# Kernel tuning notes

Hardware: AMD Instinct MI355X
Metric: run time of the kernel (lower is better)

Reference implementation:

```python
import jax, jax.numpy as jnp
import numpy as np

H = 16      # query heads
KV = 8      # kv heads
D = 128     # head_dim
HID = 2048  # hidden_size
T = 2048    # tokens
EPS = 1e-6
THETA = 1000000.0


def setup_inputs() -> dict:
    key = jax.random.key(0)
    ks = jax.random.split(key, 4)
    return {
        "hidden_states": jax.random.normal(ks[0], (T, HID), jnp.float32),
        "positions": jnp.arange(T, dtype=jnp.int32),
        "qkv_w": jax.random.normal(ks[1], (H * D + 2 * KV * D, HID), jnp.float32) * 0.02,
        "o_w": jax.random.normal(ks[2], (HID, H * D), jnp.float32) * 0.02,
        "q_norm_w": jnp.ones((D,), jnp.float32),
        "k_norm_w": jnp.ones((D,), jnp.float32),
    }


def _rmsnorm(x, w):
    # x: [T, heads, D]; normalize over last dim
    var = jnp.mean(x * x, axis=-1, keepdims=True)
    return x * jax.lax.rsqrt(var + EPS) * w


def _rope(x, positions):
    # neox-style rotate-half; x: [T, heads, D]
    half = D // 2
    inv_freq = 1.0 / (THETA ** (jnp.arange(0, half, dtype=jnp.float32) / half * 1.0))
    inv_freq = 1.0 / (THETA ** (jnp.arange(0, D, 2, dtype=jnp.float32) / D))
    ang = positions.astype(jnp.float32)[:, None] * inv_freq  # [T, D/2]
    cos = jnp.cos(ang)[:, None, :]
    sin = jnp.sin(ang)[:, None, :]
    x1, x2 = x[..., :half], x[..., half:]
    return jnp.concatenate([x1 * cos - x2 * sin, x2 * cos + x1 * sin], axis=-1)


def reference(hidden_states, positions, qkv_w, o_w, q_norm_w, k_norm_w):
    scale = D ** -0.5
    qkv = hidden_states @ qkv_w.T  # [T, H*D + 2*KV*D]
    q = qkv[:, : H * D].reshape(T, H, D)
    k = qkv[:, H * D : H * D + KV * D].reshape(T, KV, D)
    v = qkv[:, H * D + KV * D :].reshape(T, KV, D)

    q = _rope(_rmsnorm(q, q_norm_w), positions)
    k = _rope(_rmsnorm(k, k_norm_w), positions)

    # GQA: repeat kv heads to match query heads
    rep = H // KV
    k = jnp.repeat(k, rep, axis=1)  # [T, H, D]
    v = jnp.repeat(v, rep, axis=1)

    scores = jnp.einsum("thd,shd->hts", q, k) * scale  # [H, T, T]
    causal = positions[:, None] >= positions[None, :]  # [T, T]
    scores = jnp.where(causal[None, :, :], scores, jnp.float32(-1e30))
    p = jax.nn.softmax(scores, axis=-1)
    o = jnp.einsum("hts,shd->thd", p, v).reshape(T, H * D)
    return o @ o_w.T  # [T, HID]
```

## Files before the change

kernel.cpp:

```cpp
#include <hip/hip_runtime.h>
#include <math.h>

#define T_TOK 2048
#define HID 2048
#define NH 16
#define NKV 8
#define HD 128
#define QKV_N 4096
#define EPS 1e-6f

typedef unsigned short u16;
typedef unsigned int   u32;
typedef __attribute__((ext_vector_type(8))) u16   u16x8;
typedef __attribute__((ext_vector_type(8))) short short8;
typedef __attribute__((ext_vector_type(4))) float floatx4;
typedef __attribute__((ext_vector_type(16))) float f32x16;
typedef __attribute__((ext_vector_type(4))) u32   u32x4;

__device__ __forceinline__ u16 f2bf(float x) {
    u32 u = __float_as_uint(x);
    u = (u + 0x7fffu + ((u >> 16) & 1u)) >> 16;
    return (u16)u;
}
__device__ __forceinline__ float bf2f(u16 h) {
    return __uint_as_float(((u32)h) << 16);
}
__device__ __forceinline__ u32 cvtpk_bf16(float lo, float hi) {
    u32 r;
    asm("v_cvt_pk_bf16_f32 %0, %1, %2" : "=v"(r) : "v"(lo), "v"(hi));
    return r;
}

__device__ __forceinline__ void cvt8(const float* __restrict__ in,
                                     u16* __restrict__ out, size_t i)
{
    float4 a = *(const float4*)(in + i);
    float4 b = *(const float4*)(in + i + 4);
    u16x8 o;
    o[0] = f2bf(a.x); o[1] = f2bf(a.y); o[2] = f2bf(a.z); o[3] = f2bf(a.w);
    o[4] = f2bf(b.x); o[5] = f2bf(b.y); o[6] = f2bf(b.z); o[7] = f2bf(b.w);
    *(u16x8*)(out + i) = o;
}

__global__ __launch_bounds__(256) void cvt_pair(
    const float* __restrict__ ina, u16* __restrict__ outa,
    const float* __restrict__ inb, u16* __restrict__ outb)
{
    const int bid = blockIdx.x;
    if (bid < 2048) cvt8(ina, outa, ((size_t)bid * 256 + threadIdx.x) * 8);
    else            cvt8(inb, outb, ((size_t)(bid - 2048) * 256 + threadIdx.x) * 8);
}

#define GBM 256
#define GBN 128
#define GBK 64
#define BUFSH 24576

#define WAITV6 asm volatile("s_waitcnt vmcnt(6)" ::: "memory")
#define WAITV0 asm volatile("s_waitcnt vmcnt(0)" ::: "memory")
#define LGKM0  asm volatile("s_waitcnt lgkmcnt(0)" ::: "memory")
#define BARR   asm volatile("s_barrier" ::: "memory")
#define SB     __builtin_amdgcn_sched_barrier(0)

#define STAGEU(i, tt, dstb) \
    __builtin_amdgcn_global_load_lds( \
        (const __attribute__((address_space(1))) u32*)(gsrc[i] + (size_t)(tt)*GBK), \
        (__attribute__((address_space(3))) u32*)((dstb) + loff[i]), 16, 0, 0)

#define RD_A(dst, srcb, f) do { \
    dst[0] = *(const short8*)((srcb) + arow + (f)*1024 + achunk0); \
    dst[1] = *(const short8*)((srcb) + arow + (f)*1024 + achunk1); } while (0)

#define RD_B(dst, srcb) do { \
    _Pragma("unroll") \
    for (int j_ = 0; j_ < 4; ++j_) { \
        dst[j_][0] = *(const short8*)((srcb) + 16384 + brow + j_*1024 + achunk0); \
        dst[j_][1] = *(const short8*)((srcb) + 16384 + brow + j_*1024 + achunk1); } } while (0)

#define MM(f, aa, bb) do { \
    __builtin_amdgcn_s_setprio(1); \
    _Pragma("unroll") \
    for (int j_ = 0; j_ < 4; ++j_) { \
        acc[f][j_] = __builtin_amdgcn_mfma_f32_16x16x32_bf16(aa[0], bb[j_][0], acc[f][j_], 0, 0, 0); \
        acc[f][j_] = __builtin_amdgcn_mfma_f32_16x16x32_bf16(aa[1], bb[j_][1], acc[f][j_], 0, 0, 0); } \
    __builtin_amdgcn_s_setprio(0); } while (0)

#define TILE(t, CURB, NXTB, THDB, BBC, BBN) do { \
    const bool st_ = (t) + 2 < nt; \
    if (st_) { STAGEU(0, (t)+2, THDB); STAGEU(1, (t)+2, THDB); } \
    RD_A(aP1, CURB, 1); SB; \
    MM(0, aP0, BBC); SB; \
    if (st_) { STAGEU(2, (t)+2, THDB); STAGEU(3, (t)+2, THDB); } \
    RD_A(aP0, CURB, 2); SB; \
    MM(1, aP1, BBC); SB; \
    if (st_) { STAGEU(4, (t)+2, THDB); STAGEU(5, (t)+2, THDB); } \
    RD_A(aP1, CURB, 3); SB; \
    MM(2, aP0, BBC); \
    if ((t) + 1 < nt) { \
        if (st_) { WAITV6; } else { WAITV0; } \
        LGKM0; BARR; SB; \
        RD_B(BBN, NXTB); RD_A(aP0, NXTB, 0); \
    } \
    SB; \
    MM(3, aP1, BBC); SB; \
} while (0)

template<bool OUT_BF16>
__global__ __launch_bounds__(512, 2) void gemm_bt_8p(
    const u16* __restrict__ A, const u16* __restrict__ B,
    void* __restrict__ Cv, int K, int lda, int ldb, int ldc)
{
    extern __shared__ short lds[];
    const int tid = threadIdx.x;
    const int w  = tid >> 6;
    const int l  = tid & 63;
    const int m0 = blockIdx.y * GBM;
    const int n0 = blockIdx.x * GBN;
    const int mr = (w >> 1) * 64;
    const int nc = (w & 1) * 64;
    const int cc = l & 15;
    const int q4 = l >> 4;

    const int lr = l >> 3;
    const int gchunk = ((l & 7) ^ (lr & 7)) * 8;
    const u16* gsrc[6]; int loff[6];
    #pragma unroll
    for (int i = 0; i < 6; ++i) {
        const int u = w * 6 + i;
        if (u < 32) {
            gsrc[i] = A + (size_t)(m0 + u*8 + lr) * lda + gchunk;
            loff[i] = u * 512;
        } else {
            const int v = u - 32;
            gsrc[i] = B + (size_t)(n0 + v*8 + lr) * ldb + gchunk;
            loff[i] = 16384 + v * 512;
        }
    }

    const int achunk0 = ((q4)     ^ (cc & 7)) * 8;
    const int achunk1 = ((4 + q4) ^ (cc & 7)) * 8;
    const int arow = (mr + cc) * 64;
    const int brow = (nc + cc) * 64;

    floatx4 acc[4][4];
    #pragma unroll
    for (int f = 0; f < 4; ++f)
        #pragma unroll
        for (int j = 0; j < 4; ++j) acc[f][j] = (floatx4){0.f, 0.f, 0.f, 0.f};

    short8 aP0[2], aP1[2], bbE[4][2], bbO[4][2];
    short* b0 = lds;
    short* b1 = lds + BUFSH;
    short* b2 = lds + 2 * BUFSH;
    const int nt = K >> 6;

    #pragma unroll
    for (int i = 0; i < 6; ++i) STAGEU(i, 0, b0);
    #pragma unroll
    for (int i = 0; i < 6; ++i) STAGEU(i, 1, b1);
    WAITV6; BARR; SB;
    RD_B(bbE, b0); RD_A(aP0, b0, 0);

    short *CURB = b0, *NXTB = b1, *THDB = b2;
    for (int t = 0; t < nt; t += 2) {
        TILE(t, CURB, NXTB, THDB, bbE, bbO);
        { short* tmp = CURB; CURB = NXTB; NXTB = THDB; THDB = tmp; }
        TILE(t + 1, CURB, NXTB, THDB, bbO, bbE);
        { short* tmp = CURB; CURB = NXTB; NXTB = THDB; THDB = tmp; }
    }

    const int r0 = q4 * 4;
    #pragma unroll
    for (int f = 0; f < 4; ++f)
        #pragma unroll
        for (int j = 0; j < 4; ++j)
            #pragma unroll
            for (int r = 0; r < 4; ++r) {
                const int row = m0 + mr + f*16 + r0 + r;
                const int col = n0 + nc + j*16 + cc;
                if (OUT_BF16)
                    ((u16*)Cv)[(size_t)row * ldc + col] = f2bf(acc[f][j][r]);
                else
                    ((float*)Cv)[(size_t)row * ldc + col] = acc[f][j][r];
            }
}

__global__ __launch_bounds__(256) void prep_cvt(
    u16* __restrict__ qkv, const int* __restrict__ positions,
    const float* __restrict__ qw, const float* __restrict__ kw,
    u16* __restrict__ Kp, u16* __restrict__ Vtp,
    const float* __restrict__ ow, u16* __restrict__ owbf)
{
    const int bid = blockIdx.x;
    if (bid >= 256) {
        cvt8(ow, owbf, ((size_t)(bid - 256) * 256 + threadIdx.x) * 8);
        return;
    }
    const int tile = bid & 31, kvh = bid >> 5;
    const int tid = threadIdx.x;
    const int w = tid >> 6, l = tid & 63;
    const int t0 = tile * 64;

    const float qw0 = qw[2*l], qw1 = qw[2*l+1];
    const float kw0 = kw[2*l], kw1 = kw[2*l+1];
    const int   i0  = (2*l) & 63;
    const float if0 = exp2f(-(float)i0     * 0.311430758895690f);
    const float if1 = exp2f(-(float)(i0+1) * 0.311430758895690f);

    for (int rr = w; rr < 64; rr += 4) {
        const int t = t0 + rr;
        const int pos = positions[t];
        const float a0 = (float)pos * if0;
        const float a1 = (float)pos * if1;
        const float s0 = sinf(a0), c0 = cosf(a0);
        const float s1 = sinf(a1), c1 = cosf(a1);

        #pragma unroll
        for (int pass = 0; pass < 3; ++pass) {
            const int off = (pass < 2) ? (2*kvh + pass)*HD : NH*HD + kvh*HD;
            const float w0 = (pass < 2) ? qw0 : kw0;
            const float w1 = (pass < 2) ? qw1 : kw1;
            u16* p = qkv + (size_t)t*QKV_N + off;

            const u32 pk = *(const u32*)(p + 2*l);
            const float x0 = bf2f((u16)pk), x1 = bf2f((u16)(pk >> 16));
            float ss = x0*x0 + x1*x1;
            #pragma unroll
            for (int x = 1; x < 64; x <<= 1) ss += __shfl_xor(ss, x);
            const float rs = rsqrtf(ss * (1.0f/128.0f) + EPS);
            const float xn0 = x0 * rs * w0, xn1 = x1 * rs * w1;
            const float px0 = __shfl_xor(xn0, 32);
            const float px1 = __shfl_xor(xn1, 32);

            float o0, o1;
            if (l < 32) { o0 = xn0*c0 - px0*s0; o1 = xn1*c1 - px1*s1; }
            else        { o0 = xn0*c0 + px0*s0; o1 = xn1*c1 + px1*s1; }
            const u32 outpk = (u32)f2bf(o0) | ((u32)f2bf(o1) << 16);

            if (pass < 2) {
                *(u32*)(p + 2*l) = outpk;
            } else {
                const int ch = l >> 2;
                u16* dst = Kp + ((size_t)(kvh*32 + tile)*64 + rr)*128
                              + (ch ^ (rr & 15))*8 + (l & 3)*2;
                *(u32*)dst = outpk;
            }
        }
    }

    __shared__ u16 tl[64][136];
    {
        const int t  = tid >> 2;
        const int c0 = (tid & 3) * 32;
        const u16* src = qkv + (size_t)(t0 + t)*QKV_N + NH*HD + NKV*HD + kvh*HD + c0;
        #pragma unroll
        for (int p2 = 0; p2 < 4; ++p2)
            *(u16x8*)(&tl[t][c0 + p2*8]) = *(const u16x8*)(src + p2*8);
    }
    __syncthreads();
    {
        u16* dstb = Vtp + (size_t)(kvh*32 + tile) * 128 * 64;
        #pragma unroll
        for (int i = 0; i < 4; ++i) {
            const int id = tid*4 + i;
            const int d = id >> 3;
            const int o = id & 7;
            const int sb = (o ^ (d & 7)) * 8;
            u16x8 v;
            #pragma unroll
            for (int j = 0; j < 8; ++j) v[j] = tl[sb + j][d];
            *(u16x8*)(dstb + d*64 + o*8) = v;
        }
    }
}

__global__ __launch_bounds__(256, 2) void attn_mfma32(
    const u16* __restrict__ qkv, const u16* __restrict__ Kp,
    const u16* __restrict__ Vtp,
    u16* __restrict__ Opart, float2* __restrict__ ml)
{
    const int id   = blockIdx.x;
    const int kvh  = id & 7;
    const int u    = id >> 3;
    const int half = u >> 5;
    const int v    = u & 31;
    const int hp   = v & 1;
    const int bq   = v >> 1;
    const int qt   = half ? bq : 15 - bq;
    const int h    = kvh*2 + hp;
    const int t0q  = qt * 128;

    const int tid = threadIdx.x;
    const int w   = tid >> 6;
    const int l   = tid & 63;
    const int q31 = l & 31;
    const int hi  = l >> 5;

    __shared__ short Ks[2][8192];
    __shared__ short Vts[2][8192];

    short8 qf[8];
    {
        const u16* qrow = qkv + (size_t)(t0q + w*32 + q31) * QKV_N + h*HD;
        #pragma unroll
        for (int ks = 0; ks < 8; ++ks)
            qf[ks] = *(const short8*)(qrow + ks*16 + hi*8);
    }

    float m_run = -3.0e38f, l_run = 0.f;
    f32x16 accO[4];
    #pragma unroll
    for (int nd = 0; nd < 4; ++nd)
        #pragma unroll
        for (int r = 0; r < 16; ++r) accO[nd][r] = 0.f;

    const float Cs = 0.12751744f;

    const int nt  = 2*qt + 2;
    const int nh0 = qt + 1;
    const int tlo = half ? nh0 : 0;
    const int thi = half ? nt  : nh0;

    auto issue = [&](int tile, int buf) {
        const size_t tb = (size_t)(kvh*32 + tile) * 8192;
        const u16* g = ((w < 2) ? Kp : Vtp) + tb + (w & 1)*4096 + l*8;
        short* p = ((w < 2) ? Ks[buf] : Vts[buf]) + (w & 1)*4096 + l*8;
        #pragma unroll
        for (int i = 0; i < 8; ++i)
            __builtin_amdgcn_global_load_lds(
                (const __attribute__((address_space(1))) u32*)(g + i*512),
                (__attribute__((address_space(3))) u32*)(p + i*512), 16, 0, 0);
    };

    issue(tlo, 0);
    int cur = 0;

    for (int tile = tlo; tile < thi; ++tile) {
        __syncthreads();
        if (tile + 1 < thi) issue(tile + 1, cur ^ 1);

        const short* Kc = Ks[cur];
        const short* Vc = Vts[cur];

        f32x16 accS0, accS1;
        #pragma unroll
        for (int r = 0; r < 16; ++r) { accS0[r] = 0.f; accS1[r] = 0.f; }

        __builtin_amdgcn_s_setprio(1);
        #pragma unroll
        for (int ks = 0; ks < 8; ++ks) {
            const int pc = ((2*ks + hi) ^ (q31 & 15)) * 8;
            short8 a0 = *(const short8*)(Kc + q31*128 + pc);
            short8 a1 = *(const short8*)(Kc + (32 + q31)*128 + pc);
            accS0 = __builtin_amdgcn_mfma_f32_32x32x16_bf16(a0, qf[ks], accS0, 0, 0, 0);
            accS1 = __builtin_amdgcn_mfma_f32_32x32x16_bf16(a1, qf[ks], accS1, 0, 0, 0);
        }
        __builtin_amdgcn_s_setprio(0);

        if (tile >= 2*qt) {
            const int qg = w*32 + q31 + t0q - tile*64;
            #pragma unroll
            for (int r = 0; r < 16; ++r) {
                const int kvb = (r&3) + 8*(r>>2) + (hi<<2);
                if (kvb > qg)      accS0[r] = -1.0e30f;
                if (kvb + 32 > qg) accS1[r] = -1.0e30f;
            }
        }

        float mx = accS0[0];
        #pragma unroll
        for (int r = 1; r < 16; ++r) mx = fmaxf(mx, accS0[r]);
        #pragma unroll
        for (int r = 0; r < 16; ++r) mx = fmaxf(mx, accS1[r]);
        mx = fmaxf(mx, __shfl_xor(mx, 32));

        if (__any(mx > m_run + 11.76f)) {
            const float m_new = fmaxf(m_run, mx);
            const float alpha = exp2f((m_run - m_new) * Cs);
            l_run *= alpha;
            m_run = m_new;
            #pragma unroll
            for (int r = 0; r < 16; ++r) {
                const float ar = __shfl(alpha, ((r&3) + 8*(r>>2)) + (hi<<2));
                accO[0][r] *= ar; accO[1][r] *= ar;
                accO[2][r] *= ar; accO[3][r] *= ar;
            }
        }

        const float mb = m_run * Cs;
        float lsum = 0.f;
        #pragma unroll
        for (int r = 0; r < 16; ++r) {
            const float e0 = exp2f(accS0[r]*Cs - mb);
            const float e1 = exp2f(accS1[r]*Cs - mb);
            accS0[r] = e0; accS1[r] = e1;
            lsum += e0 + e1;
        }
        lsum += __shfl_xor(lsum, 32);
        l_run += lsum;

        __builtin_amdgcn_s_setprio(1);
        #pragma unroll
        for (int ks = 0; ks < 4; ++ks) {
            const int R = (ks & 1) * 8;
            u32 x0, x1, x2, x3;
            if (ks < 2) {
                x0 = cvtpk_bf16(accS0[R+0], accS0[R+1]);
                x1 = cvtpk_bf16(accS0[R+2], accS0[R+3]);
                x2 = cvtpk_bf16(accS0[R+4], accS0[R+5]);
                x3 = cvtpk_bf16(accS0[R+6], accS0[R+7]);
            } else {
                x0 = cvtpk_bf16(accS1[R+0], accS1[R+1]);
                x1 = cvtpk_bf16(accS1[R+2], accS1[R+3]);
                x2 = cvtpk_bf16(accS1[R+4], accS1[R+5]);
                x3 = cvtpk_bf16(accS1[R+6], accS1[R+7]);
            }
            asm("v_permlane32_swap_b32 %0, %1" : "+v"(x0), "+v"(x2));
            asm("v_permlane32_swap_b32 %0, %1" : "+v"(x1), "+v"(x3));
            u32x4 aw; aw.x = x0; aw.y = x1; aw.z = x2; aw.w = x3;
            const short8 aP = __builtin_bit_cast(short8, aw);
            #pragma unroll
            for (int nd = 0; nd < 4; ++nd) {
                short8 bv = *(const short8*)(Vc + (nd*32 + q31)*64
                                             + ((2*ks + hi) ^ (q31 & 7))*8);
                accO[nd] = __builtin_amdgcn_mfma_f32_32x32x16_bf16(aP, bv, accO[nd], 0, 0, 0);
            }
        }
        __builtin_amdgcn_s_setprio(0);

        cur ^= 1;
    }

    const size_t pbase = (size_t)(half * NH + h) * T_TOK;
    #pragma unroll
    for (int r = 0; r < 16; ++r) {
        const int qr = (r&3) + 8*(r>>2) + (hi<<2);
        u16* op = Opart + (pbase + t0q + w*32 + qr) * HD;
        op[q31]      = f2bf(accO[0][r]);
        op[32 + q31] = f2bf(accO[1][r]);
        op[64 + q31] = f2bf(accO[2][r]);
        op[96 + q31] = f2bf(accO[3][r]);
    }
    if (l < 32)
        ml[pbase + t0q + w*32 + l] = make_float2(m_run, l_run);
}

__global__ __launch_bounds__(256) void attn_combine(
    const u16* __restrict__ Opart, const float2* __restrict__ ml,
    u16* __restrict__ qkv)
{
    const int idx = blockIdx.x * 256 + threadIdx.x;
    const int c16 = idx & 15;
    const int t   = (idx >> 4) & (T_TOK - 1);
    const int h   = idx >> 15;
    const size_t iA = (size_t)h * T_TOK + t;
    const size_t iB = (size_t)(NH + h) * T_TOK + t;
    const float2 a = ml[iA];
    const float2 b = ml[iB];
    const float Cs = 0.12751744f;
    const float mM = fmaxf(a.x, b.x);
    const float wA = exp2f((a.x - mM) * Cs);
    const float wB = exp2f((b.x - mM) * Cs);
    const float inv = 1.0f / (wA * a.y + wB * b.y);
    const u16x8 A = *(const u16x8*)(Opart + iA * HD + c16*8);
    const u16x8 B = *(const u16x8*)(Opart + iB * HD + c16*8);
    u16x8 o;
    #pragma unroll
    for (int j = 0; j < 8; ++j)
        o[j] = f2bf((wA * bf2f(A[j]) + wB * bf2f(B[j])) * inv);
    *(u16x8*)(qkv + (size_t)t * QKV_N + h * HD + c16*8) = o;
}

extern "C" void kernel_launch(void* const* d_in, const int* in_sizes, int n_in,
                              void* d_out, int out_size, void* d_ws, size_t ws_size,
                              hipStream_t stream)
{
    const float* hidden    = (const float*)d_in[0];
    const int*   positions = (const int*)  d_in[1];
    const float* qkv_w     = (const float*)d_in[2];
    const float* o_w       = (const float*)d_in[3];
    const float* q_norm_w  = (const float*)d_in[4];
    const float* k_norm_w  = (const float*)d_in[5];
    float* out = (float*)d_out;

    u16* qkvbf = (u16*)d_ws;
    u16* wbf   = qkvbf + (size_t)T_TOK * QKV_N;
    u16* abf   = wbf   + (size_t)QKV_N * HID;
    u16* kpb   = abf   + (size_t)T_TOK * HID;
    u16* vpb   = kpb   + (size_t)NKV * T_TOK * HD;

    static bool s_attr = false;
    if (!s_attr) {
        (void)hipFuncSetAttribute(
            reinterpret_cast<const void*>(&gemm_bt_8p<true>),
            hipFuncAttributeMaxDynamicSharedMemorySize, 147456);
        (void)hipFuncSetAttribute(
            reinterpret_cast<const void*>(&gemm_bt_8p<false>),
            hipFuncAttributeMaxDynamicSharedMemorySize, 147456);
        s_attr = true;
    }

    cvt_pair<<<6144, 256, 0, stream>>>(hidden, abf, qkv_w, wbf);

    gemm_bt_8p<true><<<dim3(QKV_N/GBN, T_TOK/GBM), 512, 147456, stream>>>(
        abf, wbf, qkvbf, HID, HID, HID, QKV_N);

    prep_cvt<<<2304, 256, 0, stream>>>(
        qkvbf, positions, q_norm_w, k_norm_w, kpb, vpb, o_w, abf);

    attn_mfma32<<<512, 256, 0, stream>>>(qkvbf, kpb, vpb, wbf, (float2*)out);

    attn_combine<<<(NH*T_TOK*16)/256, 256, 0, stream>>>(
        wbf, (const float2*)out, qkvbf);

    gemm_bt_8p<false><<<dim3(HID/GBN, T_TOK/GBM), 512, 147456, stream>>>(
        qkvbf, abf, out, HID, QKV_N, HID, HID);
}
```

Baseline: 240.0 us.

## Use 256-row query tiles with four-way KV split and fused 4-way combine

The attention kernel now gives each wave two 32-row query groups (256 query rows per block), so every K fragment loaded from LDS feeds two MFMAs. Each query tile's KV range is split into four equal parts instead of two halves, which keeps the block count at 512 with balanced work. The combine step now merges four partials and also carries the o_w bf16 conversion, which moves out of prep. Partial buffers are placed in reused workspace and output memory. The trade-off is roughly double the accumulator registers and more partial traffic.

```diff
diff --git a/kernel.cpp b/kernel.cpp
--- a/kernel.cpp
+++ b/kernel.cpp
@@ -185,17 +185,12 @@
             }
 }
 
-__global__ __launch_bounds__(256) void prep_cvt(
+__global__ __launch_bounds__(256) void prep(
     u16* __restrict__ qkv, const int* __restrict__ positions,
     const float* __restrict__ qw, const float* __restrict__ kw,
-    u16* __restrict__ Kp, u16* __restrict__ Vtp,
-    const float* __restrict__ ow, u16* __restrict__ owbf)
+    u16* __restrict__ Kp, u16* __restrict__ Vtp)
 {
     const int bid = blockIdx.x;
-    if (bid >= 256) {
-        cvt8(ow, owbf, ((size_t)(bid - 256) * 256 + threadIdx.x) * 8);
-        return;
-    }
     const int tile = bid & 31, kvh = bid >> 5;
     const int tid = threadIdx.x;
     const int w = tid >> 6, l = tid & 63;
@@ -277,18 +272,21 @@
 __global__ __launch_bounds__(256, 2) void attn_mfma32(
     const u16* __restrict__ qkv, const u16* __restrict__ Kp,
     const u16* __restrict__ Vtp,
-    u16* __restrict__ Opart, float2* __restrict__ ml)
+    u16* __restrict__ P0, u16* __restrict__ P1,
+    u16* __restrict__ P2, u16* __restrict__ P3,
+    float2* __restrict__ ml)
 {
     const int id   = blockIdx.x;
     const int kvh  = id & 7;
     const int u    = id >> 3;
-    const int half = u >> 5;
-    const int v    = u & 31;
-    const int hp   = v & 1;
-    const int bq   = v >> 1;
-    const int qt   = half ? bq : 15 - bq;
+    const int b5   = u >> 5;
+    const int r5   = u & 31;
+    const int hp   = r5 & 1;
+    const int part = (r5 >> 1) & 3;
+    const int q3   = r5 >> 3;
+    const int qt   = b5 ? 7 - q3 : q3;
     const int h    = kvh*2 + hp;
-    const int t0q  = qt * 128;
+    const int t0q  = qt * 256;
 
     const int tid = threadIdx.x;
     const int w   = tid >> 6;
@@ -299,27 +297,28 @@
     __shared__ short Ks[2][8192];
     __shared__ short Vts[2][8192];
 
-    short8 qf[8];
-    {
-        const u16* qrow = qkv + (size_t)(t0q + w*32 + q31) * QKV_N + h*HD;
+    short8 qf[2][8];
+    #pragma unroll
+    for (int qg = 0; qg < 2; ++qg) {
+        const u16* qrow = qkv + (size_t)(t0q + w*64 + qg*32 + q31) * QKV_N + h*HD;
         #pragma unroll
         for (int ks = 0; ks < 8; ++ks)
-            qf[ks] = *(const short8*)(qrow + ks*16 + hi*8);
-    }
-
-    float m_run = -3.0e38f, l_run = 0.f;
-    f32x16 accO[4];
-    #pragma unroll
-    for (int nd = 0; nd < 4; ++nd)
-        #pragma unroll
-        for (int r = 0; r < 16; ++r) accO[nd][r] = 0.f;
+            qf[qg][ks] = *(const short8*)(qrow + ks*16 + hi*8);
+    }
+
+    float m_run[2] = {-3.0e38f, -3.0e38f}, l_run[2] = {0.f, 0.f};
+    f32x16 accO[2][4];
+    #pragma unroll
+    for (int qg = 0; qg < 2; ++qg)
+        #pragma unroll
+        for (int nd = 0; nd < 4; ++nd)
+            #pragma unroll
+            for (int r = 0; r < 16; ++r) accO[qg][nd][r] = 0.f;
 
     const float Cs = 0.12751744f;
 
-    const int nt  = 2*qt + 2;
-    const int nh0 = qt + 1;
-    const int tlo = half ? nh0 : 0;
-    const int thi = half ? nt  : nh0;
+    const int tlo = part * (qt + 1);
+    const int thi = tlo + (qt + 1);
 
     auto issue = [&](int tile, int buf) {
         const size_t tb = (size_t)(kvh*32 + tile) * 8192;
@@ -335,139 +334,158 @@
     issue(tlo, 0);
     int cur = 0;
 
-    for (int tile = tlo; tile < thi; ++tile) {
+    for (int tt = tlo; tt < thi; ++tt) {
         __syncthreads();
-        if (tile + 1 < thi) issue(tile + 1, cur ^ 1);
+        if (tt + 1 < thi) issue(tt + 1, cur ^ 1);
 
         const short* Kc = Ks[cur];
         const short* Vc = Vts[cur];
 
-        f32x16 accS0, accS1;
-        #pragma unroll
-        for (int r = 0; r < 16; ++r) { accS0[r] = 0.f; accS1[r] = 0.f; }
-
-        __builtin_amdgcn_s_setprio(1);
-        #pragma unroll
-        for (int ks = 0; ks < 8; ++ks) {
-            const int pc = ((2*ks + hi) ^ (q31 & 15)) * 8;
-            short8 a0 = *(const short8*)(Kc + q31*128 + pc);
-            short8 a1 = *(const short8*)(Kc + (32 + q31)*128 + pc);
-            accS0 = __builtin_amdgcn_mfma_f32_32x32x16_bf16(a0, qf[ks], accS0, 0, 0, 0);
-            accS1 = __builtin_amdgcn_mfma_f32_32x32x16_bf16(a1, qf[ks], accS1, 0, 0, 0);
+        #pragma unroll
+        for (int sub = 0; sub < 2; ++sub) {
+            f32x16 accS[2];
+            #pragma unroll
+            for (int r = 0; r < 16; ++r) { accS[0][r] = 0.f; accS[1][r] = 0.f; }
+
+            __builtin_amdgcn_s_setprio(1);
+            #pragma unroll
+            for (int ks = 0; ks < 8; ++ks) {
+                short8 a = *(const short8*)(Kc + (sub*32 + q31)*128
+                                            + ((2*ks + hi) ^ (q31 & 15))*8);
+                accS[0] = __builtin_amdgcn_mfma_f32_32x32x16_bf16(a, qf[0][ks], accS[0], 0, 0, 0);
+                accS[1] = __builtin_amdgcn_mfma_f32_32x32x16_bf16(a, qf[1][ks], accS[1], 0, 0, 0);
+            }
+            __builtin_amdgcn_s_setprio(0);
+
+            if (tt >= 4*qt) {
+                const int kvb0 = tt*64 + sub*32 + (hi<<2);
+                #pragma unroll
+                for (int qg = 0; qg < 2; ++qg) {
+                    const int qg_g = t0q + w*64 + qg*32 + q31;
+                    #pragma unroll
+                    for (int r = 0; r < 16; ++r) {
+                        const int kvg = kvb0 + (r&3) + 8*(r>>2);
+                        if (kvg > qg_g) accS[qg][r] = -1.0e30f;
+                    }
+                }
+            }
+
+            #pragma unroll
+            for (int qg = 0; qg < 2; ++qg) {
+                float mx = accS[qg][0];
+                #pragma unroll
+                for (int r = 1; r < 16; ++r) mx = fmaxf(mx, accS[qg][r]);
+                mx = fmaxf(mx, __shfl_xor(mx, 32));
+
+                if (__any(mx > m_run[qg] + 11.76f)) {
+                    const float m_new = fmaxf(m_run[qg], mx);
+                    const float alpha = exp2f((m_run[qg] - m_new) * Cs);
+                    l_run[qg] *= alpha;
+                    m_run[qg] = m_new;
+                    #pragma unroll
+                    for (int r = 0; r < 16; ++r) {
+                        const float ar = __shfl(alpha, ((r&3) + 8*(r>>2)) + (hi<<2));
+                        accO[qg][0][r] *= ar; accO[qg][1][r] *= ar;
+                        accO[qg][2][r] *= ar; accO[qg][3][r] *= ar;
+                    }
+                }
+                const float mb = m_run[qg] * Cs;
+                float lsum = 0.f;
+                #pragma unroll
+                for (int r = 0; r < 16; ++r) {
+                    const float e = exp2f(accS[qg][r]*Cs - mb);
+                    accS[qg][r] = e;
+                    lsum += e;
+                }
+                lsum += __shfl_xor(lsum, 32);
+                l_run[qg] += lsum;
+            }
+
+            __builtin_amdgcn_s_setprio(1);
+            #pragma unroll
+            for (int ks2 = 0; ks2 < 2; ++ks2) {
+                const int R = ks2 * 8;
+                short8 aP[2];
+                #pragma unroll
+                for (int qg = 0; qg < 2; ++qg) {
+                    u32 x0 = cvtpk_bf16(accS[qg][R+0], accS[qg][R+1]);
+                    u32 x1 = cvtpk_bf16(accS[qg][R+2], accS[qg][R+3]);
+                    u32 x2 = cvtpk_bf16(accS[qg][R+4], accS[qg][R+5]);
+                    u32 x3 = cvtpk_bf16(accS[qg][R+6], accS[qg][R+7]);
+                    asm("v_permlane32_swap_b32 %0, %1" : "+v"(x0), "+v"(x2));
+                    asm("v_permlane32_swap_b32 %0, %1" : "+v"(x1), "+v"(x3));
+                    u32x4 aw; aw.x = x0; aw.y = x1; aw.z = x2; aw.w = x3;
+                    aP[qg] = __builtin_bit_cast(short8, aw);
+                }
+                const int ksg = sub*2 + ks2;
+                #pragma unroll
+                for (int nd = 0; nd < 4; ++nd) {
+                    short8 bv = *(const short8*)(Vc + (nd*32 + q31)*64
+                                                 + ((2*ksg + hi) ^ (q31 & 7))*8);
+                    accO[0][nd] = __builtin_amdgcn_mfma_f32_32x32x16_bf16(aP[0], bv, accO[0][nd], 0, 0, 0);
+                    accO[1][nd] = __builtin_amdgcn_mfma_f32_32x32x16_bf16(aP[1], bv, accO[1][nd], 0, 0, 0);
+                }
+            }
+            __builtin_amdgcn_s_setprio(0);
         }
-        __builtin_amdgcn_s_setprio(0);
-
-        if (tile >= 2*qt) {
-            const int qg = w*32 + q31 + t0q - tile*64;
-            #pragma unroll
-            for (int r = 0; r < 16; ++r) {
-                const int kvb = (r&3) + 8*(r>>2) + (hi<<2);
-                if (kvb > qg)      accS0[r] = -1.0e30f;
-                if (kvb + 32 > qg) accS1[r] = -1.0e30f;
-            }
+        cur ^= 1;
+    }
+
+    u16* Op = (part == 0) ? P0 : (part == 1) ? P1 : (part == 2) ? P2 : P3;
+    const size_t hb = (size_t)h * T_TOK;
+    #pragma unroll
+    for (int qg = 0; qg < 2; ++qg) {
+        #pragma unroll
+        for (int r = 0; r < 16; ++r) {
+            const int qr = (r&3) + 8*(r>>2) + (hi<<2);
+            u16* op = Op + (hb + t0q + w*64 + qg*32 + qr) * HD;
+            op[q31]      = f2bf(accO[qg][0][r]);
+            op[32 + q31] = f2bf(accO[qg][1][r]);
+            op[64 + q31] = f2bf(accO[qg][2][r]);
+            op[96 + q31] = f2bf(accO[qg][3][r]);
         }
-
-        float mx = accS0[0];
-        #pragma unroll
-        for (int r = 1; r < 16; ++r) mx = fmaxf(mx, accS0[r]);
-        #pragma unroll
-        for (int r = 0; r < 16; ++r) mx = fmaxf(mx, accS1[r]);
-        mx = fmaxf(mx, __shfl_xor(mx, 32));
-
-        if (__any(mx > m_run + 11.76f)) {
-            const float m_new = fmaxf(m_run, mx);
-            const float alpha = exp2f((m_run - m_new) * Cs);
-            l_run *= alpha;
-            m_run = m_new;
-            #pragma unroll
-            for (int r = 0; r < 16; ++r) {
-                const float ar = __shfl(alpha, ((r&3) + 8*(r>>2)) + (hi<<2));
-                accO[0][r] *= ar; accO[1][r] *= ar;
-                accO[2][r] *= ar; accO[3][r] *= ar;
-            }
-        }
-
-        const float mb = m_run * Cs;
-        float lsum = 0.f;
-        #pragma unroll
-        for (int r = 0; r < 16; ++r) {
-            const float e0 = exp2f(accS0[r]*Cs - mb);
-            const float e1 = exp2f(accS1[r]*Cs - mb);
-            accS0[r] = e0; accS1[r] = e1;
-            lsum += e0 + e1;
-        }
-        lsum += __shfl_xor(lsum, 32);
-        l_run += lsum;
-
-        __builtin_amdgcn_s_setprio(1);
-        #pragma unroll
-        for (int ks = 0; ks < 4; ++ks) {
-            const int R = (ks & 1) * 8;
-            u32 x0, x1, x2, x3;
-            if (ks < 2) {
-                x0 = cvtpk_bf16(accS0[R+0], accS0[R+1]);
-                x1 = cvtpk_bf16(accS0[R+2], accS0[R+3]);
-                x2 = cvtpk_bf16(accS0[R+4], accS0[R+5]);
-                x3 = cvtpk_bf16(accS0[R+6], accS0[R+7]);
-            } else {
-                x0 = cvtpk_bf16(accS1[R+0], accS1[R+1]);
-                x1 = cvtpk_bf16(accS1[R+2], accS1[R+3]);
-                x2 = cvtpk_bf16(accS1[R+4], accS1[R+5]);
-                x3 = cvtpk_bf16(accS1[R+6], accS1[R+7]);
-            }
-            asm("v_permlane32_swap_b32 %0, %1" : "+v"(x0), "+v"(x2));
-            asm("v_permlane32_swap_b32 %0, %1" : "+v"(x1), "+v"(x3));
-            u32x4 aw; aw.x = x0; aw.y = x1; aw.z = x2; aw.w = x3;
-            const short8 aP = __builtin_bit_cast(short8, aw);
-            #pragma unroll
-            for (int nd = 0; nd < 4; ++nd) {
-                short8 bv = *(const short8*)(Vc + (nd*32 + q31)*64
-                                             + ((2*ks + hi) ^ (q31 & 7))*8);
-                accO[nd] = __builtin_amdgcn_mfma_f32_32x32x16_bf16(aP, bv, accO[nd], 0, 0, 0);
-            }
-        }
-        __builtin_amdgcn_s_setprio(0);
-
-        cur ^= 1;
-    }
-
-    const size_t pbase = (size_t)(half * NH + h) * T_TOK;
-    #pragma unroll
-    for (int r = 0; r < 16; ++r) {
-        const int qr = (r&3) + 8*(r>>2) + (hi<<2);
-        u16* op = Opart + (pbase + t0q + w*32 + qr) * HD;
-        op[q31]      = f2bf(accO[0][r]);
-        op[32 + q31] = f2bf(accO[1][r]);
-        op[64 + q31] = f2bf(accO[2][r]);
-        op[96 + q31] = f2bf(accO[3][r]);
-    }
-    if (l < 32)
-        ml[pbase + t0q + w*32 + l] = make_float2(m_run, l_run);
-}
-
-__global__ __launch_bounds__(256) void attn_combine(
-    const u16* __restrict__ Opart, const float2* __restrict__ ml,
-    u16* __restrict__ qkv)
-{
-    const int idx = blockIdx.x * 256 + threadIdx.x;
+        if (l < 32)
+            ml[(size_t)part*NH*T_TOK + hb + t0q + w*64 + qg*32 + l]
+                = make_float2(m_run[qg], l_run[qg]);
+    }
+}
+
+__global__ __launch_bounds__(256) void combine4_cvt(
+    const u16* __restrict__ P0, const u16* __restrict__ P1,
+    const u16* __restrict__ P2, const u16* __restrict__ P3,
+    const float2* __restrict__ ml, u16* __restrict__ qkv,
+    const float* __restrict__ ow, u16* __restrict__ owbf)
+{
+    const int bid = blockIdx.x;
+    if (bid >= 2048) {
+        cvt8(ow, owbf, ((size_t)(bid - 2048) * 256 + threadIdx.x) * 8);
+        return;
+    }
+    const int idx = bid * 256 + threadIdx.x;
     const int c16 = idx & 15;
     const int t   = (idx >> 4) & (T_TOK - 1);
     const int h   = idx >> 15;
-    const size_t iA = (size_t)h * T_TOK + t;
-    const size_t iB = (size_t)(NH + h) * T_TOK + t;
-    const float2 a = ml[iA];
-    const float2 b = ml[iB];
+    const size_t base = (size_t)h * T_TOK + t;
+    const size_t NT = (size_t)NH * T_TOK;
+    const float2 a = ml[base];
+    const float2 b = ml[base + NT];
+    const float2 c = ml[base + 2*NT];
+    const float2 d = ml[base + 3*NT];
     const float Cs = 0.12751744f;
-    const float mM = fmaxf(a.x, b.x);
+    const float mM = fmaxf(fmaxf(a.x, b.x), fmaxf(c.x, d.x));
     const float wA = exp2f((a.x - mM) * Cs);
     const float wB = exp2f((b.x - mM) * Cs);
-    const float inv = 1.0f / (wA * a.y + wB * b.y);
-    const u16x8 A = *(const u16x8*)(Opart + iA * HD + c16*8);
-    const u16x8 B = *(const u16x8*)(Opart + iB * HD + c16*8);
+    const float wC = exp2f((c.x - mM) * Cs);
+    const float wD = exp2f((d.x - mM) * Cs);
+    const float inv = 1.0f / (wA*a.y + wB*b.y + wC*c.y + wD*d.y);
+    const u16x8 A = *(const u16x8*)(P0 + base * HD + c16*8);
+    const u16x8 B = *(const u16x8*)(P1 + base * HD + c16*8);
+    const u16x8 C = *(const u16x8*)(P2 + base * HD + c16*8);
+    const u16x8 D = *(const u16x8*)(P3 + base * HD + c16*8);
     u16x8 o;
     #pragma unroll
     for (int j = 0; j < 8; ++j)
-        o[j] = f2bf((wA * bf2f(A[j]) + wB * bf2f(B[j])) * inv);
+        o[j] = f2bf((wA*bf2f(A[j]) + wB*bf2f(B[j]) + wC*bf2f(C[j]) + wD*bf2f(D[j])) * inv);
     *(u16x8*)(qkv + (size_t)t * QKV_N + h * HD + c16*8) = o;
 }
 
@@ -488,6 +506,12 @@
     u16* abf   = wbf   + (size_t)QKV_N * HID;
     u16* kpb   = abf   + (size_t)T_TOK * HID;
     u16* vpb   = kpb   + (size_t)NKV * T_TOK * HD;
+
+    u16* P0 = wbf;
+    u16* P1 = wbf + (size_t)NH * T_TOK * HD;
+    u16* P2 = abf;
+    u16* P3 = (u16*)out;
+    float2* mlp = (float2*)((u16*)out + (size_t)NH * T_TOK * HD);
 
     static bool s_attr = false;
     if (!s_attr) {
@@ -505,14 +529,12 @@
     gemm_bt_8p<true><<<dim3(QKV_N/GBN, T_TOK/GBM), 512, 147456, stream>>>(
         abf, wbf, qkvbf, HID, HID, HID, QKV_N);
 
-    prep_cvt<<<2304, 256, 0, stream>>>(
-        qkvbf, positions, q_norm_w, k_norm_w, kpb, vpb, o_w, abf);
-
-    attn_mfma32<<<512, 256, 0, stream>>>(qkvbf, kpb, vpb, wbf, (float2*)out);
-
-    attn_combine<<<(NH*T_TOK*16)/256, 256, 0, stream>>>(
-        wbf, (const float2*)out, qkvbf);
+    prep<<<256, 256, 0, stream>>>(qkvbf, positions, q_norm_w, k_norm_w, kpb, vpb);
+
+    attn_mfma32<<<512, 256, 0, stream>>>(qkvbf, kpb, vpb, P0, P1, P2, P3, mlp);
+
+    combine4_cvt<<<4096, 256, 0, stream>>>(P0, P1, P2, P3, mlp, qkvbf, o_w, kpb);
 
     gemm_bt_8p<false><<<dim3(HID/GBN, T_TOK/GBM), 512, 147456, stream>>>(
-        qkvbf, abf, out, HID, QKV_N, HID, HID);
-}
+        qkvbf, kpb, out, HID, QKV_N, HID, HID);
+}
```

Result: slower. 268.6 us (+11.9%).
